# Optimization experiments

Measured on AMD Instinct MI355X. Metric: run time of the kernel, lower is better.

## Reference

```python
import jax, jax.numpy as jnp
import numpy as np
from math import sqrt

H = 16  # head_num


def setup_inputs() -> dict:
    key = jax.random.key(0)
    ks = jax.random.split(key, 8)
    B, Sq, Skv, Dq, Dkv, Dall = 2, 2048, 2048, 1024, 1024, 1024
    x = jax.random.normal(ks[0], (B, Sq, Dq), dtype=jnp.float32)
    y = jax.random.normal(ks[1], (B, Skv, Dkv), dtype=jnp.float32)
    attention_mask = jnp.ones((B, 1, Sq, Skv), dtype=jnp.int32)
    # torch nn.Linear weights are [out, in]
    Wq = jax.random.normal(ks[2], (Dall, Dq), dtype=jnp.float32) * 0.02
    Wk = jax.random.normal(ks[3], (Dall, Dkv), dtype=jnp.float32) * 0.02
    Wv = jax.random.normal(ks[4], (Dall, Dkv), dtype=jnp.float32) * 0.02
    Wo = jax.random.normal(ks[5], (Dq, Dall), dtype=jnp.float32) * 0.02
    bo = jnp.zeros((Dq,), dtype=jnp.float32)
    return {"x": x, "y": y, "attention_mask": attention_mask,
            "Wq": Wq, "Wk": Wk, "Wv": Wv, "Wo": Wo, "bo": bo}


def reference(x, y, attention_mask, Wq, Wk, Wv, Wo, bo):
    B, Sq, _ = x.shape
    Dall = Wq.shape[0]
    Dh = Dall // H
    # projections (torch Linear: x @ W.T), split heads -> [B, H, S, Dh]
    q = (x @ Wq.T).reshape(B, Sq, H, Dh).transpose(0, 2, 1, 3)
    k = (y @ Wk.T).reshape(B, -1, H, Dh).transpose(0, 2, 1, 3)
    v = (y @ Wv.T).reshape(B, -1, H, Dh).transpose(0, 2, 1, 3)
    scores = jnp.einsum('bhqd,bhkd->bhqk', q, k)  # [B,H,Sq,Skv]
    mask = (attention_mask == 0)  # masked_fill where mask.eq(0) -> but torch does mask.eq(0) then fills True positions
    scores = jnp.where(mask, jnp.float32(-1e9), scores)
    # NOTE: faithful quirk - mask applied before scaling; scale uses sqrt(h_size)
    attn = jax.nn.softmax(scores / sqrt(Dh), axis=-1)
    out = jnp.einsum('bhqk,bhkd->bhqd', attn, v)
    out = out.transpose(0, 2, 1, 3).reshape(B, Sq, Dall)
    return out @ Wo.T + bo
```

## Files before the change

kernel.cpp:

```cpp
#include <hip/hip_runtime.h>
#include <stdint.h>


typedef __attribute__((ext_vector_type(8))) short bf16x8;
typedef __attribute__((ext_vector_type(4))) float f32x4;
typedef __attribute__((ext_vector_type(16))) float f32x16;
typedef __attribute__((ext_vector_type(2))) unsigned int u32x2;

#define LOG2E 1.44269504088896f
#define QSCALE (0.125f * LOG2E)

static __device__ __forceinline__ unsigned short f2bf(float f) {
  union { float f; unsigned int u; } v; v.f = f;
  unsigned int r = v.u + 0x7FFFu + ((v.u >> 16) & 1u);
  return (unsigned short)(r >> 16);
}

static __device__ __forceinline__ void g2l16(const void* gsrc, void* ldst) {
  __builtin_amdgcn_global_load_lds((const __attribute__((address_space(1))) unsigned int*)gsrc,
                                   (__attribute__((address_space(3))) unsigned int*)ldst,
                                   16, 0, 0);
}

static __device__ __forceinline__ unsigned int cvt_pk_bf16(float lo, float hi) {
  unsigned int r;
  asm("v_cvt_pk_bf16_f32 %0, %1, %2" : "=v"(r) : "v"(lo), "v"(hi));
  return r;
}

static __device__ __forceinline__ u32x2 pl32swap(unsigned int a, unsigned int b) {
  return __builtin_amdgcn_permlane32_swap(a, b, false, false);
}

static __device__ __forceinline__ f32x16 mfma32(bf16x8 a, bf16x8 b, f32x16 c) {
  return __builtin_amdgcn_mfma_f32_32x32x16_bf16(a, b, c, 0, 0, 0);
}

static __device__ __forceinline__ size_t kfrag_addr(int row, int col) {
  int b = row >> 11, s = row & 2047;
  int h = col >> 6, d = col & 63;
  int t32 = s >> 5, r31 = s & 31;
  int ks = d >> 4, r5 = (d >> 3) & 1, e = d & 7;
  return (size_t)(b * 16 + h) * 131072 + (size_t)t32 * 2048 + ks * 512 + (r5 * 32 + r31) * 8 + e;
}
static __device__ __forceinline__ size_t vfrag_addr(int row, int col) {
  int b = row >> 11, s = row & 2047;
  int h = col >> 6, d = col & 63;
  int t64 = s >> 6, k2 = (s >> 4) & 3, r5 = (s >> 3) & 1, e = s & 7;
  int mb = d >> 5, r31 = d & 31;
  return (size_t)(b * 16 + h) * 131072 + (size_t)t64 * 4096 + (mb * 4 + k2) * 512 + (r5 * 32 + r31) * 8 + e;
}

__global__ void k_prep(const float* __restrict__ x, const float* __restrict__ y,
                       const float* __restrict__ Wq, const float* __restrict__ Wk,
                       const float* __restrict__ Wv, const float* __restrict__ Wo,
                       const int* __restrict__ mask,
                       unsigned short* __restrict__ xb, unsigned short* __restrict__ yb,
                       unsigned short* __restrict__ Wqb, unsigned short* __restrict__ Wkb,
                       unsigned short* __restrict__ Wvb, unsigned short* __restrict__ Wob,
                       unsigned long long* __restrict__ bits, unsigned int* __restrict__ flag) {
  const int task = blockIdx.y;
  if (task == 6) {
    const int lane = threadIdx.x & 63;
    int gw = blockIdx.x * 4 + (threadIdx.x >> 6);
    bool any0 = false;
    for (; gw < 131072; gw += 4096) {
      int m = mask[(size_t)gw * 64 + lane];
      unsigned long long bal = __ballot(m != 0);
      if (lane == 0) {
        bits[gw] = bal;
        any0 |= (bal != ~0ull);
      }
    }
    if (lane == 0 && any0) atomicAnd(flag, 0u);
    return;
  }
  const float* in; unsigned short* out; int n;
  switch (task) {
    case 0: in = x;  out = xb;  n = 4194304; break;
    case 1: in = y;  out = yb;  n = 4194304; break;
    case 2: in = Wq; out = Wqb; n = 1048576; break;
    case 3: in = Wk; out = Wkb; n = 1048576; break;
    case 4: in = Wv; out = Wvb; n = 1048576; break;
    default: in = Wo; out = Wob; n = 1048576; break;
  }
  int i = (blockIdx.x * blockDim.x + threadIdx.x) * 4;
  const int stride = gridDim.x * blockDim.x * 4;
  for (; i < n; i += stride) {
    float4 v = *reinterpret_cast<const float4*>(in + i);
    ushort4 o;
    o.x = f2bf(v.x); o.y = f2bf(v.y); o.z = f2bf(v.z); o.w = f2bf(v.w);
    *reinterpret_cast<ushort4*>(out + i) = o;
  }
}

template <int OM>
static __device__ __forceinline__ void gemm_body(const unsigned short* __restrict__ A,
                                                 const unsigned short* __restrict__ W,
                                                 void* __restrict__ Cout,
                                                 const float* __restrict__ bias,
                                                 float scale) {
  __shared__ __align__(16) unsigned short As[128 * 32];
  __shared__ __align__(16) unsigned short Bs[128 * 32];
  const int tid = threadIdx.x;
  const int w = tid >> 6, lane = tid & 63;
  const int wr = w >> 1, wc = w & 1;
  const int l15 = lane & 15, lg = lane >> 4;
  const int bm = blockIdx.x, bn = blockIdx.y;

  f32x4 acc[4][4] = {};

  const int e0 = w * 1024 + lane * 8;
  const int e1 = e0 + 512;
  const int r0 = e0 >> 5, c0 = e0 & 31;
  const int r1 = e1 >> 5, c1 = e1 & 31;
  const unsigned short* A0 = A + (size_t)(bm * 128 + r0) * 1024 + c0;
  const unsigned short* A1 = A + (size_t)(bm * 128 + r1) * 1024 + c1;
  const unsigned short* W0 = W + (size_t)(bn * 128 + r0) * 1024 + c0;
  const unsigned short* W1 = W + (size_t)(bn * 128 + r1) * 1024 + c1;

  for (int kt = 0; kt < 1024; kt += 32) {
    g2l16(A0 + kt, (char*)As + e0 * 2);
    g2l16(A1 + kt, (char*)As + e1 * 2);
    g2l16(W0 + kt, (char*)Bs + e0 * 2);
    g2l16(W1 + kt, (char*)Bs + e1 * 2);
    __syncthreads();
    bf16x8 a[4], b[4];
#pragma unroll
    for (int mi = 0; mi < 4; ++mi)
      a[mi] = *reinterpret_cast<const bf16x8*>(As + (wr * 64 + mi * 16 + l15) * 32 + lg * 8);
#pragma unroll
    for (int ni = 0; ni < 4; ++ni)
      b[ni] = *reinterpret_cast<const bf16x8*>(Bs + (wc * 64 + ni * 16 + l15) * 32 + lg * 8);
#pragma unroll
    for (int mi = 0; mi < 4; ++mi)
#pragma unroll
      for (int ni = 0; ni < 4; ++ni)
        acc[mi][ni] = __builtin_amdgcn_mfma_f32_16x16x32_bf16(a[mi], b[ni], acc[mi][ni], 0, 0, 0);
    __syncthreads();
  }

#pragma unroll
  for (int ni = 0; ni < 4; ++ni) {
    const int gcol = bn * 128 + wc * 64 + ni * 16 + l15;
    float bv = (OM == 1) ? bias[gcol] : 0.f;
#pragma unroll
    for (int mi = 0; mi < 4; ++mi) {
#pragma unroll
      for (int r = 0; r < 4; ++r) {
        const int grow = bm * 128 + wr * 64 + mi * 16 + lg * 4 + r;
        if (OM == 0)
          ((unsigned short*)Cout)[(size_t)grow * 1024 + gcol] = f2bf(acc[mi][ni][r]);
        else if (OM == 1)
          ((float*)Cout)[(size_t)grow * 1024 + gcol] = acc[mi][ni][r] + bv;
        else if (OM == 2)
          ((unsigned short*)Cout)[kfrag_addr(grow, gcol)] = f2bf(acc[mi][ni][r] * scale);
        else
          ((unsigned short*)Cout)[vfrag_addr(grow, gcol)] = f2bf(acc[mi][ni][r]);
      }
    }
  }
}

__global__ __launch_bounds__(256) void k_gemm_qkv(
    const unsigned short* __restrict__ xb, const unsigned short* __restrict__ yb,
    const unsigned short* __restrict__ Wq, const unsigned short* __restrict__ Wk,
    const unsigned short* __restrict__ Wv,
    unsigned short* __restrict__ Qf, unsigned short* __restrict__ Kf,
    unsigned short* __restrict__ Vf) {
  const int z = blockIdx.z;
  if (z == 0) gemm_body<2>(xb, Wq, Qf, nullptr, QSCALE);
  else if (z == 1) gemm_body<2>(yb, Wk, Kf, nullptr, 1.f);
  else gemm_body<3>(yb, Wv, Vf, nullptr, 1.f);
}

__global__ __launch_bounds__(256) void k_gemm_o(
    const unsigned short* __restrict__ AO, const unsigned short* __restrict__ Wo,
    float* __restrict__ out, const float* __restrict__ bo) {
  gemm_body<1>(AO, Wo, out, bo, 1.f);
}


#define BUILD_PB2(SP, K2, IDX) {                                   \
    unsigned int c0_ = cvt_pk_bf16(SP[(K2)*8 + 0], SP[(K2)*8 + 1]);\
    unsigned int c1_ = cvt_pk_bf16(SP[(K2)*8 + 2], SP[(K2)*8 + 3]);\
    unsigned int c2_ = cvt_pk_bf16(SP[(K2)*8 + 4], SP[(K2)*8 + 5]);\
    unsigned int c3_ = cvt_pk_bf16(SP[(K2)*8 + 6], SP[(K2)*8 + 7]);\
    u32x2 r0_ = pl32swap(c0_, c2_);                                \
    u32x2 r1_ = pl32swap(c1_, c3_);                                \
    union { unsigned int u[4]; bf16x8 v; } f_;                     \
    f_.u[0] = r0_.x; f_.u[1] = r1_.x; f_.u[2] = r0_.y; f_.u[3] = r1_.y; \
    pb[IDX] = f_.v; }

#define STAGE_TILE(T, BUF) {                                                  \
    const size_t toff_ = (size_t)(T) * 8192;                                  \
    char* kb_ = smem + (BUF) * 16384;                                         \
    const int o0_ = (w * 2 + 0) * 1024 + lane * 16;                           \
    const int o1_ = (w * 2 + 1) * 1024 + lane * 16;                           \
    g2l16(Kg + toff_ + o0_, kb_ + o0_);                                       \
    g2l16(Kg + toff_ + o1_, kb_ + o1_);                                       \
    g2l16(Vg + toff_ + o0_, kb_ + 8192 + o0_);                                \
    g2l16(Vg + toff_ + o1_, kb_ + 8192 + o1_);                                \
  }

__global__ __launch_bounds__(256, 2) void k_attn(
    const unsigned short* __restrict__ Qf, const unsigned short* __restrict__ Kf,
    const unsigned short* __restrict__ Vf, const unsigned long long* __restrict__ bits,
    const unsigned int* __restrict__ flag, unsigned short* __restrict__ AO) {
  __shared__ __align__(16) char smem[32768];
  const int tid = threadIdx.x, w = tid >> 6, lane = tid & 63;
  const int l31 = lane & 31, hi = lane >> 5;
  const int bid = blockIdx.x;
  const int xcd = bid & 7, rr = bid >> 3;
  const int j = rr & 15;
  const int g = xcd + ((rr >> 4) << 3);
  const int h = g & 15, b = g >> 4;
  const int q = j * 128 + w * 32 + l31;
  const bool allfull = (*flag == 0xFFFFFFFFu);
  const f32x16 z16 = {};

  const size_t bh = (size_t)(b * 16 + h) * 131072;
  bf16x8 qf[4];
  const unsigned short* Qp = Qf + bh + (size_t)(j * 4 + w) * 2048 + lane * 8;
#pragma unroll
  for (int ks = 0; ks < 4; ++ks)
    qf[ks] = *reinterpret_cast<const bf16x8*>(Qp + ks * 512);

  const char* Kg = (const char*)(Kf + bh);
  const char* Vg = (const char*)(Vf + bh);
  const unsigned long long* brow = bits + (size_t)(b * 2048 + q) * 32;

  f32x16 o0 = {}, o1 = {};
  float l_run = 0.f;

  STAGE_TILE(0, 0)
  __syncthreads();

  for (int t = 0; t < 32; ++t) {
    const int cur = t & 1;
    if (t < 31) STAGE_TILE(t + 1, cur ^ 1)
    const char* Kb = smem + cur * 16384;
    const char* Vb = Kb + 8192;

    bf16x8 kf[8], vf[8];
#pragma unroll
    for (int f = 0; f < 8; ++f)
      kf[f] = *reinterpret_cast<const bf16x8*>(Kb + f * 1024 + lane * 16);

    f32x16 s0 = z16, s1 = z16;
#pragma unroll
    for (int ks = 0; ks < 4; ++ks) {
      s0 = mfma32(kf[ks], qf[ks], s0);
      s1 = mfma32(kf[4 + ks], qf[ks], s1);
    }

#pragma unroll
    for (int f = 0; f < 8; ++f)
      vf[f] = *reinterpret_cast<const bf16x8*>(Vb + f * 1024 + lane * 16);

    if (!allfull) {
      unsigned long long wb = brow[t];
      if (!__all(wb == ~0ull)) {
#pragma unroll
        for (int r = 0; r < 16; ++r) {
          const int kl = (r & 3) + 8 * (r >> 2) + 4 * hi;
          s0[r] = ((wb >> kl) & 1ull) ? s0[r] : -1e9f;
          s1[r] = ((wb >> (kl + 32)) & 1ull) ? s1[r] : -1e9f;
        }
      }
    }

#pragma unroll
    for (int r = 0; r < 16; ++r) {
      s0[r] = __builtin_amdgcn_exp2f(s0[r]);
      s1[r] = __builtin_amdgcn_exp2f(s1[r]);
    }
    {
      float sm[8];
#pragma unroll
      for (int r = 0; r < 8; ++r) sm[r] = (s0[r] + s0[r + 8]) + (s1[r] + s1[r + 8]);
      sm[0] += sm[4]; sm[1] += sm[5]; sm[2] += sm[6]; sm[3] += sm[7];
      sm[0] += sm[2]; sm[1] += sm[3];
      float ls = sm[0] + sm[1];
      u32x2 sw = pl32swap(__builtin_bit_cast(unsigned int, ls),
                          __builtin_bit_cast(unsigned int, ls));
      l_run += __builtin_bit_cast(float, sw.x) + __builtin_bit_cast(float, sw.y);
    }

    bf16x8 pb[4];
    BUILD_PB2(s0, 0, 0) BUILD_PB2(s0, 1, 1) BUILD_PB2(s1, 0, 2) BUILD_PB2(s1, 1, 3)
#pragma unroll
    for (int k2 = 0; k2 < 4; ++k2) {
      o0 = mfma32(vf[k2], pb[k2], o0);
      o1 = mfma32(vf[4 + k2], pb[k2], o1);
    }
    __syncthreads();
  }

  const float inv = 1.f / l_run;
  unsigned short* Orow = AO + (size_t)(b * 2048 + q) * 1024 + h * 64;
#pragma unroll
  for (int g2 = 0; g2 < 4; ++g2) {
    ushort4 pk;
    pk.x = f2bf(o0[g2 * 4 + 0] * inv);
    pk.y = f2bf(o0[g2 * 4 + 1] * inv);
    pk.z = f2bf(o0[g2 * 4 + 2] * inv);
    pk.w = f2bf(o0[g2 * 4 + 3] * inv);
    *reinterpret_cast<ushort4*>(Orow + 8 * g2 + 4 * hi) = pk;
    pk.x = f2bf(o1[g2 * 4 + 0] * inv);
    pk.y = f2bf(o1[g2 * 4 + 1] * inv);
    pk.z = f2bf(o1[g2 * 4 + 2] * inv);
    pk.w = f2bf(o1[g2 * 4 + 3] * inv);
    *reinterpret_cast<ushort4*>(Orow + 32 + 8 * g2 + 4 * hi) = pk;
  }
}

extern "C" void kernel_launch(void* const* d_in, const int* in_sizes, int n_in,
                              void* d_out, int out_size, void* d_ws, size_t ws_size,
                              hipStream_t stream) {
  const float* x  = (const float*)d_in[0];
  const float* y  = (const float*)d_in[1];
  const int* mask = (const int*)d_in[2];
  const float* Wq = (const float*)d_in[3];
  const float* Wk = (const float*)d_in[4];
  const float* Wv = (const float*)d_in[5];
  const float* Wo = (const float*)d_in[6];
  const float* bo = (const float*)d_in[7];

  char* ws = (char*)d_ws;
  const size_t MB = 1ull << 20;
  unsigned short* xb  = (unsigned short*)(ws + 0 * MB);
  unsigned short* yb  = (unsigned short*)(ws + 8 * MB);
  unsigned short* Wqb = (unsigned short*)(ws + 16 * MB);
  unsigned short* Wkb = (unsigned short*)(ws + 18 * MB);
  unsigned short* Wvb = (unsigned short*)(ws + 20 * MB);
  unsigned short* Wob = (unsigned short*)(ws + 22 * MB);
  unsigned short* Qf  = (unsigned short*)(ws + 24 * MB);
  unsigned short* Kf  = (unsigned short*)(ws + 32 * MB);
  unsigned short* Vf  = (unsigned short*)(ws + 40 * MB);
  unsigned short* AOb = (unsigned short*)(ws + 56 * MB);
  unsigned long long* bits = (unsigned long long*)(ws + 64 * MB);
  unsigned int* flag = (unsigned int*)(ws + 65 * MB);

  hipMemsetAsync(flag, 0xFF, 4, stream);
  k_prep<<<dim3(1024, 7), 256, 0, stream>>>(x, y, Wq, Wk, Wv, Wo, mask,
                                            xb, yb, Wqb, Wkb, Wvb, Wob, bits, flag);
  k_gemm_qkv<<<dim3(32, 8, 3), 256, 0, stream>>>(xb, yb, Wqb, Wkb, Wvb, Qf, Kf, Vf);
  k_attn<<<512, 256, 0, stream>>>(Qf, Kf, Vf, bits, flag, AOb);
  k_gemm_o<<<dim3(32, 8, 1), 256, 0, stream>>>(AOb, Wob, (float*)d_out, bo);
}
```

Baseline: 131.1 us.

## Use 128-key attention stages with MFMA priority and smaller-tile output GEMM

```diff
diff --git a/kernel.cpp b/kernel.cpp
--- a/kernel.cpp
+++ b/kernel.cpp
@@ -98,7 +98,6 @@
 static __device__ __forceinline__ void gemm_body(const unsigned short* __restrict__ A,
                                                  const unsigned short* __restrict__ W,
                                                  void* __restrict__ Cout,
-                                                 const float* __restrict__ bias,
                                                  float scale) {
   __shared__ __align__(16) unsigned short As[128 * 32];
   __shared__ __align__(16) unsigned short Bs[128 * 32];
@@ -143,17 +142,12 @@
 #pragma unroll
   for (int ni = 0; ni < 4; ++ni) {
     const int gcol = bn * 128 + wc * 64 + ni * 16 + l15;
-    float bv = (OM == 1) ? bias[gcol] : 0.f;
 #pragma unroll
     for (int mi = 0; mi < 4; ++mi) {
 #pragma unroll
       for (int r = 0; r < 4; ++r) {
         const int grow = bm * 128 + wr * 64 + mi * 16 + lg * 4 + r;
-        if (OM == 0)
-          ((unsigned short*)Cout)[(size_t)grow * 1024 + gcol] = f2bf(acc[mi][ni][r]);
-        else if (OM == 1)
-          ((float*)Cout)[(size_t)grow * 1024 + gcol] = acc[mi][ni][r] + bv;
-        else if (OM == 2)
+        if (OM == 2)
           ((unsigned short*)Cout)[kfrag_addr(grow, gcol)] = f2bf(acc[mi][ni][r] * scale);
         else
           ((unsigned short*)Cout)[vfrag_addr(grow, gcol)] = f2bf(acc[mi][ni][r]);
@@ -169,15 +163,66 @@
     unsigned short* __restrict__ Qf, unsigned short* __restrict__ Kf,
     unsigned short* __restrict__ Vf) {
   const int z = blockIdx.z;
-  if (z == 0) gemm_body<2>(xb, Wq, Qf, nullptr, QSCALE);
-  else if (z == 1) gemm_body<2>(yb, Wk, Kf, nullptr, 1.f);
-  else gemm_body<3>(yb, Wv, Vf, nullptr, 1.f);
+  if (z == 0) gemm_body<2>(xb, Wq, Qf, QSCALE);
+  else if (z == 1) gemm_body<2>(yb, Wk, Kf, 1.f);
+  else gemm_body<3>(yb, Wv, Vf, 1.f);
 }
 
 __global__ __launch_bounds__(256) void k_gemm_o(
-    const unsigned short* __restrict__ AO, const unsigned short* __restrict__ Wo,
+    const unsigned short* __restrict__ A, const unsigned short* __restrict__ W,
     float* __restrict__ out, const float* __restrict__ bo) {
-  gemm_body<1>(AO, Wo, out, bo, 1.f);
+  __shared__ __align__(16) unsigned short As[64 * 32];
+  __shared__ __align__(16) unsigned short Bs[128 * 32];
+  const int tid = threadIdx.x;
+  const int w = tid >> 6, lane = tid & 63;
+  const int l15 = lane & 15, lg = lane >> 4;
+  const int bm = blockIdx.x, bn = blockIdx.y;
+
+  f32x4 acc[4][2] = {};
+
+  const int ea = tid * 8;
+  const int eb0 = tid * 8;
+  const int eb1 = eb0 + 2048;
+  const int ra = ea >> 5, ca = ea & 31;
+  const int rb0 = eb0 >> 5, cb0 = eb0 & 31;
+  const int rb1 = eb1 >> 5, cb1 = eb1 & 31;
+  const unsigned short* A0 = A + (size_t)(bm * 64 + ra) * 1024 + ca;
+  const unsigned short* W0 = W + (size_t)(bn * 128 + rb0) * 1024 + cb0;
+  const unsigned short* W1 = W + (size_t)(bn * 128 + rb1) * 1024 + cb1;
+
+  for (int kt = 0; kt < 1024; kt += 32) {
+    g2l16(A0 + kt, (char*)As + ea * 2);
+    g2l16(W0 + kt, (char*)Bs + eb0 * 2);
+    g2l16(W1 + kt, (char*)Bs + eb1 * 2);
+    __syncthreads();
+    bf16x8 a[4], b[2];
+#pragma unroll
+    for (int mi = 0; mi < 4; ++mi)
+      a[mi] = *reinterpret_cast<const bf16x8*>(As + (mi * 16 + l15) * 32 + lg * 8);
+#pragma unroll
+    for (int ni = 0; ni < 2; ++ni)
+      b[ni] = *reinterpret_cast<const bf16x8*>(Bs + (w * 32 + ni * 16 + l15) * 32 + lg * 8);
+#pragma unroll
+    for (int mi = 0; mi < 4; ++mi)
+#pragma unroll
+      for (int ni = 0; ni < 2; ++ni)
+        acc[mi][ni] = __builtin_amdgcn_mfma_f32_16x16x32_bf16(a[mi], b[ni], acc[mi][ni], 0, 0, 0);
+    __syncthreads();
+  }
+
+#pragma unroll
+  for (int ni = 0; ni < 2; ++ni) {
+    const int gcol = bn * 128 + w * 32 + ni * 16 + l15;
+    const float bv = bo[gcol];
+#pragma unroll
+    for (int mi = 0; mi < 4; ++mi) {
+#pragma unroll
+      for (int r = 0; r < 4; ++r) {
+        const int grow = bm * 64 + mi * 16 + lg * 4 + r;
+        out[(size_t)grow * 1024 + gcol] = acc[mi][ni][r] + bv;
+      }
+    }
+  }
 }
 
 
@@ -192,22 +237,80 @@
     f_.u[0] = r0_.x; f_.u[1] = r1_.x; f_.u[2] = r0_.y; f_.u[3] = r1_.y; \
     pb[IDX] = f_.v; }
 
-#define STAGE_TILE(T, BUF) {                                                  \
-    const size_t toff_ = (size_t)(T) * 8192;                                  \
-    char* kb_ = smem + (BUF) * 16384;                                         \
-    const int o0_ = (w * 2 + 0) * 1024 + lane * 16;                           \
-    const int o1_ = (w * 2 + 1) * 1024 + lane * 16;                           \
-    g2l16(Kg + toff_ + o0_, kb_ + o0_);                                       \
-    g2l16(Kg + toff_ + o1_, kb_ + o1_);                                       \
-    g2l16(Vg + toff_ + o0_, kb_ + 8192 + o0_);                                \
-    g2l16(Vg + toff_ + o1_, kb_ + 8192 + o1_);                                \
+#define STAGE128(T, BUF) {                                                    \
+    const char* ks_ = Kg + (size_t)(T) * 16384;                               \
+    const char* vs_ = Vg + (size_t)(T) * 16384;                               \
+    char* db_ = smem + (BUF) * 32768;                                         \
+    const int lo_ = tid * 16;                                                 \
+    _Pragma("unroll")                                                         \
+    for (int c_ = 0; c_ < 4; ++c_) {                                          \
+      g2l16(ks_ + c_ * 4096 + lo_, db_ + c_ * 4096 + lo_);                    \
+      g2l16(vs_ + c_ * 4096 + lo_, db_ + 16384 + c_ * 4096 + lo_);            \
+    }                                                                         \
+  }
+
+#define HALF_BODY(BASE, HALF, TW)                                             \
+  {                                                                           \
+    const char* Kb = (BASE) + (HALF) * 8192;                                  \
+    const char* Vb = (BASE) + 16384 + (HALF) * 8192;                          \
+    bf16x8 kf[8], vf[8];                                                      \
+    _Pragma("unroll")                                                         \
+    for (int f = 0; f < 8; ++f)                                               \
+      kf[f] = *reinterpret_cast<const bf16x8*>(Kb + f * 1024 + lane * 16);    \
+    f32x16 s0 = z16, s1 = z16;                                                \
+    __builtin_amdgcn_s_setprio(1);                                            \
+    _Pragma("unroll")                                                         \
+    for (int ks = 0; ks < 4; ++ks) {                                          \
+      s0 = mfma32(kf[ks], qf[ks], s0);                                        \
+      s1 = mfma32(kf[4 + ks], qf[ks], s1);                                    \
+    }                                                                         \
+    __builtin_amdgcn_s_setprio(0);                                            \
+    _Pragma("unroll")                                                         \
+    for (int f = 0; f < 8; ++f)                                               \
+      vf[f] = *reinterpret_cast<const bf16x8*>(Vb + f * 1024 + lane * 16);    \
+    if (!allfull) {                                                           \
+      unsigned long long wb = brow[TW];                                       \
+      if (!__all(wb == ~0ull)) {                                              \
+        _Pragma("unroll")                                                     \
+        for (int r = 0; r < 16; ++r) {                                        \
+          const int kl = (r & 3) + 8 * (r >> 2) + 4 * hi;                     \
+          s0[r] = ((wb >> kl) & 1ull) ? s0[r] : -1e9f;                        \
+          s1[r] = ((wb >> (kl + 32)) & 1ull) ? s1[r] : -1e9f;                 \
+        }                                                                     \
+      }                                                                       \
+    }                                                                         \
+    _Pragma("unroll")                                                         \
+    for (int r = 0; r < 16; ++r) {                                            \
+      s0[r] = __builtin_amdgcn_exp2f(s0[r]);                                  \
+      s1[r] = __builtin_amdgcn_exp2f(s1[r]);                                  \
+    }                                                                         \
+    {                                                                         \
+      float sm[8];                                                            \
+      _Pragma("unroll")                                                       \
+      for (int r = 0; r < 8; ++r) sm[r] = (s0[r] + s0[r + 8]) + (s1[r] + s1[r + 8]); \
+      sm[0] += sm[4]; sm[1] += sm[5]; sm[2] += sm[6]; sm[3] += sm[7];         \
+      sm[0] += sm[2]; sm[1] += sm[3];                                         \
+      float ls = sm[0] + sm[1];                                               \
+      u32x2 sw = pl32swap(__builtin_bit_cast(unsigned int, ls),               \
+                          __builtin_bit_cast(unsigned int, ls));              \
+      l_run += __builtin_bit_cast(float, sw.x) + __builtin_bit_cast(float, sw.y); \
+    }                                                                         \
+    bf16x8 pb[4];                                                             \
+    BUILD_PB2(s0, 0, 0) BUILD_PB2(s0, 1, 1) BUILD_PB2(s1, 0, 2) BUILD_PB2(s1, 1, 3) \
+    __builtin_amdgcn_s_setprio(1);                                            \
+    _Pragma("unroll")                                                         \
+    for (int k2 = 0; k2 < 4; ++k2) {                                          \
+      o0 = mfma32(vf[k2], pb[k2], o0);                                        \
+      o1 = mfma32(vf[4 + k2], pb[k2], o1);                                    \
+    }                                                                         \
+    __builtin_amdgcn_s_setprio(0);                                            \
   }
 
 __global__ __launch_bounds__(256, 2) void k_attn(
     const unsigned short* __restrict__ Qf, const unsigned short* __restrict__ Kf,
     const unsigned short* __restrict__ Vf, const unsigned long long* __restrict__ bits,
     const unsigned int* __restrict__ flag, unsigned short* __restrict__ AO) {
-  __shared__ __align__(16) char smem[32768];
+  __shared__ __align__(16) char smem[65536];
   const int tid = threadIdx.x, w = tid >> 6, lane = tid & 63;
   const int l31 = lane & 31, hi = lane >> 5;
   const int bid = blockIdx.x;
@@ -233,67 +336,15 @@
   f32x16 o0 = {}, o1 = {};
   float l_run = 0.f;
 
-  STAGE_TILE(0, 0)
+  STAGE128(0, 0)
   __syncthreads();
 
-  for (int t = 0; t < 32; ++t) {
+  for (int t = 0; t < 16; ++t) {
     const int cur = t & 1;
-    if (t < 31) STAGE_TILE(t + 1, cur ^ 1)
-    const char* Kb = smem + cur * 16384;
-    const char* Vb = Kb + 8192;
-
-    bf16x8 kf[8], vf[8];
-#pragma unroll
-    for (int f = 0; f < 8; ++f)
-      kf[f] = *reinterpret_cast<const bf16x8*>(Kb + f * 1024 + lane * 16);
-
-    f32x16 s0 = z16, s1 = z16;
-#pragma unroll
-    for (int ks = 0; ks < 4; ++ks) {
-      s0 = mfma32(kf[ks], qf[ks], s0);
-      s1 = mfma32(kf[4 + ks], qf[ks], s1);
-    }
-
-#pragma unroll
-    for (int f = 0; f < 8; ++f)
-      vf[f] = *reinterpret_cast<const bf16x8*>(Vb + f * 1024 + lane * 16);
-
-    if (!allfull) {
-      unsigned long long wb = brow[t];
-      if (!__all(wb == ~0ull)) {
-#pragma unroll
-        for (int r = 0; r < 16; ++r) {
-          const int kl = (r & 3) + 8 * (r >> 2) + 4 * hi;
-          s0[r] = ((wb >> kl) & 1ull) ? s0[r] : -1e9f;
-          s1[r] = ((wb >> (kl + 32)) & 1ull) ? s1[r] : -1e9f;
-        }
-      }
-    }
-
-#pragma unroll
-    for (int r = 0; r < 16; ++r) {
-      s0[r] = __builtin_amdgcn_exp2f(s0[r]);
-      s1[r] = __builtin_amdgcn_exp2f(s1[r]);
-    }
-    {
-      float sm[8];
-#pragma unroll
-      for (int r = 0; r < 8; ++r) sm[r] = (s0[r] + s0[r + 8]) + (s1[r] + s1[r + 8]);
-      sm[0] += sm[4]; sm[1] += sm[5]; sm[2] += sm[6]; sm[3] += sm[7];
-      sm[0] += sm[2]; sm[1] += sm[3];
-      float ls = sm[0] + sm[1];
-      u32x2 sw = pl32swap(__builtin_bit_cast(unsigned int, ls),
-                          __builtin_bit_cast(unsigned int, ls));
-      l_run += __builtin_bit_cast(float, sw.x) + __builtin_bit_cast(float, sw.y);
-    }
-
-    bf16x8 pb[4];
-    BUILD_PB2(s0, 0, 0) BUILD_PB2(s0, 1, 1) BUILD_PB2(s1, 0, 2) BUILD_PB2(s1, 1, 3)
-#pragma unroll
-    for (int k2 = 0; k2 < 4; ++k2) {
-      o0 = mfma32(vf[k2], pb[k2], o0);
-      o1 = mfma32(vf[4 + k2], pb[k2], o1);
-    }
+    if (t < 15) STAGE128(t + 1, cur ^ 1)
+    const char* base = smem + cur * 32768;
+    HALF_BODY(base, 0, 2 * t)
+    HALF_BODY(base, 1, 2 * t + 1)
     __syncthreads();
   }
 
@@ -347,5 +398,5 @@
                                             xb, yb, Wqb, Wkb, Wvb, Wob, bits, flag);
   k_gemm_qkv<<<dim3(32, 8, 3), 256, 0, stream>>>(xb, yb, Wqb, Wkb, Wvb, Qf, Kf, Vf);
   k_attn<<<512, 256, 0, stream>>>(Qf, Kf, Vf, bits, flag, AOb);
-  k_gemm_o<<<dim3(32, 8, 1), 256, 0, stream>>>(AOb, Wob, (float*)d_out, bo);
-}
+  k_gemm_o<<<dim3(64, 8), 256, 0, stream>>>(AOb, Wob, (float*)d_out, bo);
+}
```

Measured after the change: 129.4 us. About the same (-1.3%).
